# Optimization experiments

Measured on AMD Instinct MI355X. Metric: run time of the kernel, lower is better.

## Reference

```python
import jax, jax.numpy as jnp
import numpy as np

N_NODES = 50000
N_EDGES = 800000
D_IN = 128
D_H = 128
D_OUT = 1
N_GRAPHS = 64
BN_EPS = 1e-5


def _lin(key, i, o):
    return jax.random.normal(key, (i, o), jnp.float32) / np.float32(np.sqrt(i))


def setup_inputs() -> dict:
    key = jax.random.key(0)
    ks = jax.random.split(key, 40)
    inp = {}
    inp["x"] = jax.random.normal(ks[0], (N_NODES, D_IN), jnp.float32)
    inp["edge_index"] = jax.random.randint(ks[1], (2, N_EDGES), 0, N_NODES)
    inp["batch"] = jnp.sort(jax.random.randint(ks[2], (N_NODES,), 0, N_GRAPHS))
    dims = [D_IN, D_H, D_H]
    ki = 3
    for l in range(3):
        inp[f"l{l}_W1"] = _lin(ks[ki], dims[l], D_H); ki += 1
        inp[f"l{l}_b1"] = jnp.zeros((D_H,), jnp.float32)
        inp[f"l{l}_W2"] = _lin(ks[ki], D_H, D_H); ki += 1
        inp[f"l{l}_b2"] = jnp.zeros((D_H,), jnp.float32)
        inp[f"l{l}_g"] = jnp.ones((D_H,), jnp.float32)
        inp[f"l{l}_beta"] = jnp.zeros((D_H,), jnp.float32)
    inp["p_W1"] = _lin(ks[ki], D_H * 3, D_H); ki += 1
    inp["p_b1"] = jnp.zeros((D_H,), jnp.float32)
    inp["p_g"] = jnp.ones((D_H,), jnp.float32)
    inp["p_beta"] = jnp.zeros((D_H,), jnp.float32)
    inp["p_W2"] = _lin(ks[ki], D_H, D_OUT); ki += 1
    inp["p_b2"] = jnp.zeros((D_OUT,), jnp.float32)
    return inp


def _bn(h, g, b):
    # training-mode BatchNorm1d: biased batch statistics over dim 0
    m = h.mean(0)
    v = h.var(0)
    return (h - m) * (g / jnp.sqrt(v + BN_EPS)) + b


def _gin_conv(x, src, dst, W1, b1, W2, b2):
    # scatter-add neighbor aggregation: messages x[src] summed into dst
    agg = jax.ops.segment_sum(x[src], dst, num_segments=N_NODES)
    h = x + agg  # eps = 0 (GINConv default)
    h = jax.nn.relu(h @ W1 + b1)
    return h @ W2 + b2


def reference(x, edge_index, batch,
              l0_W1, l0_b1, l0_W2, l0_b2, l0_g, l0_beta,
              l1_W1, l1_b1, l1_W2, l1_b2, l1_g, l1_beta,
              l2_W1, l2_b1, l2_W2, l2_b2, l2_g, l2_beta,
              p_W1, p_b1, p_g, p_beta, p_W2, p_b2):
    src, dst = edge_index[0], edge_index[1]
    layers = [
        (l0_W1, l0_b1, l0_W2, l0_b2, l0_g, l0_beta),
        (l1_W1, l1_b1, l1_W2, l1_b2, l1_g, l1_beta),
        (l2_W1, l2_b1, l2_W2, l2_b2, l2_g, l2_beta),
    ]
    h = x
    h_list = []
    for (W1, b1, W2, b2, g, beta) in layers:
        h = _gin_conv(h, src, dst, W1, b1, W2, b2)
        h = jax.nn.relu(_bn(h, g, beta))
        # dropout: identity in eval mode
        h_list.append(h)
    # global mean pool per layer, then concat
    cnt = jax.ops.segment_sum(jnp.ones((N_NODES,), jnp.float32), batch,
                              num_segments=N_GRAPHS)
    cnt = jnp.maximum(cnt, 1.0)[:, None]
    pooled = [jax.ops.segment_sum(hh, batch, num_segments=N_GRAPHS) / cnt
              for hh in h_list]
    z = jnp.concatenate(pooled, axis=1)  # [G, 3*D_H]
    # prediction MLP: fc1 -> relu -> bn -> fc2 (dropout identity)
    z = jax.nn.relu(z @ p_W1 + p_b1)
    z = _bn(z, p_g, p_beta)
    return z @ p_W2 + p_b2  # [G, D_OUT]
```

## Files before the change

### kernel.cpp

```cpp
#include <hip/hip_runtime.h>

#define NN 50000
#define NE 800000
#define D  128
#define NG 64
#define BN_EPS 1e-5f
#define SCAN_B 196

typedef __attribute__((ext_vector_type(8))) short short8;
typedef __attribute__((ext_vector_type(4))) float f32x4;

static __device__ inline unsigned short f2bf_rn(float f) {
  unsigned u = __float_as_uint(f);
  unsigned r = (u + 0x7FFF + ((u >> 16) & 1)) >> 16;
  return (unsigned short)r;
}
static __device__ inline float bf2f(unsigned short h) {
  return __uint_as_float((unsigned)h << 16);
}

__global__ void k_hist(const int* __restrict__ dst, int* __restrict__ counts) {
  int e = blockIdx.x * blockDim.x + threadIdx.x;
  if (e < NE) atomicAdd(&counts[dst[e]], 1);
}

__global__ void k_scan1(const int* __restrict__ counts, int* __restrict__ bsum) {
  const int t = threadIdx.x;
  const int i = blockIdx.x * 256 + t;
  int v = (i < NN) ? counts[i] : 0;
  #pragma unroll
  for (int d = 32; d >= 1; d >>= 1) v += __shfl_xor(v, d, 64);
  __shared__ int ws[4];
  if ((t & 63) == 0) ws[t >> 6] = v;
  __syncthreads();
  if (t == 0) bsum[blockIdx.x] = ws[0] + ws[1] + ws[2] + ws[3];
}

__global__ void k_scan2(const int* __restrict__ bsum, int* __restrict__ boff,
                        int* __restrict__ offs) {
  const int t = threadIdx.x, lane = t & 63, w = t >> 6;
  int v = (t < SCAN_B) ? bsum[t] : 0;
  int s = v;
  #pragma unroll
  for (int d = 1; d < 64; d <<= 1) { int u = __shfl_up(s, d, 64); if (lane >= d) s += u; }
  __shared__ int ws[4];
  if (lane == 63) ws[w] = s;
  __syncthreads();
  int add = 0;
  for (int k = 0; k < w; ++k) add += ws[k];
  if (t < SCAN_B) boff[t] = add + s - v;
  if (t == SCAN_B - 1) offs[NN] = add + s;
}

__global__ void k_scan3(const int* __restrict__ counts, const int* __restrict__ boff,
                        int* __restrict__ offs) {
  const int t = threadIdx.x, lane = t & 63, w = t >> 6;
  const int i = blockIdx.x * 256 + t;
  int v = (i < NN) ? counts[i] : 0;
  int s = v;
  #pragma unroll
  for (int d = 1; d < 64; d <<= 1) { int u = __shfl_up(s, d, 64); if (lane >= d) s += u; }
  __shared__ int ws[4];
  if (lane == 63) ws[w] = s;
  __syncthreads();
  int add = 0;
  for (int k = 0; k < w; ++k) add += ws[k];
  if (i < NN) offs[i] = boff[blockIdx.x] + add + s - v;
}

__global__ void k_scatter(const int* __restrict__ src, const int* __restrict__ dst,
                          const int* __restrict__ offs, int* __restrict__ cursor,
                          int* __restrict__ esrc) {
  int e = blockIdx.x * blockDim.x + threadIdx.x;
  if (e < NE) {
    int d = dst[e];
    int p = offs[d] + atomicAdd(&cursor[d], 1);
    esrc[p] = src[e];
  }
}

__global__ void k_gbounds(const int* __restrict__ batch, int* __restrict__ gstart) {
  const int g = threadIdx.x;
  if (g > NG) return;
  int lo = 0, hi = NN;
  while (lo < hi) { int mid = (lo + hi) >> 1; if (batch[mid] < g) lo = mid + 1; else hi = mid; }
  gstart[g] = lo;
}

__global__ __launch_bounds__(256) void k_cvt(const float* __restrict__ X,
                                             unsigned long long* __restrict__ Xb) {
  const int n4 = NN * D / 4;
  for (int i = blockIdx.x * blockDim.x + threadIdx.x; i < n4; i += gridDim.x * blockDim.x) {
    float4 v = ((const float4*)X)[i];
    unsigned long long p = (unsigned long long)f2bf_rn(v.x) |
                           ((unsigned long long)f2bf_rn(v.y) << 16) |
                           ((unsigned long long)f2bf_rn(v.z) << 32) |
                           ((unsigned long long)f2bf_rn(v.w) << 48);
    Xb[i] = p;
  }
}

struct WPtrs { const float* w[6]; };
__global__ void k_prep6(WPtrs ws, short* __restrict__ wb) {
  const int widx = blockIdx.y;
  const float* __restrict__ W = ws.w[widx];
  short* __restrict__ Wh = wb + (size_t)(widx * 2) * 16384;
  short* __restrict__ Wl = Wh + 16384;
  const int idx = blockIdx.x * 256 + threadIdx.x;
  const int k = idx >> 7, c = idx & 127;
  const float v = W[idx];
  const unsigned short h = f2bf_rn(v);
  const unsigned short lo = f2bf_rn(v - bf2f(h));
  const int o = ((k >> 5) * 128 + c) * 32 + (k & 31);
  Wh[o] = (short)h;
  Wl[o] = (short)lo;
}

template<bool BN>
__global__ __launch_bounds__(256) void k_aggregate(const unsigned* __restrict__ Hb,
                                                   const int* __restrict__ offs,
                                                   const int* __restrict__ esrc,
                                                   const float* __restrict__ sums,
                                                   const float* __restrict__ sumsq,
                                                   const float* __restrict__ gw,
                                                   const float* __restrict__ beta,
                                                   unsigned* __restrict__ AGGh,
                                                   unsigned* __restrict__ AGGl) {
  const int node = blockIdx.x * 4 + (threadIdx.x >> 6);
  const int lane = threadIdx.x & 63;
  float2 sc = make_float2(1.f, 1.f), sh = make_float2(0.f, 0.f);
  if (BN) {
    const float2 s2 = ((const float2*)sums)[lane];
    const float2 q2 = ((const float2*)sumsq)[lane];
    const float2 g2 = ((const float2*)gw)[lane];
    const float2 b2 = ((const float2*)beta)[lane];
    const float mx = s2.x * (1.f / NN), my = s2.y * (1.f / NN);
    sc.x = g2.x / sqrtf(q2.x * (1.f / NN) - mx * mx + BN_EPS);
    sc.y = g2.y / sqrtf(q2.y * (1.f / NN) - my * my + BN_EPS);
    sh.x = b2.x - mx * sc.x;
    sh.y = b2.y - my * sc.y;
  }

  auto rd = [&](int r) -> float2 {
    const unsigned u = Hb[r * 64 + lane];
    float2 v = make_float2(bf2f((unsigned short)u), bf2f((unsigned short)(u >> 16)));
    if (BN) {
      v.x = fmaxf(fmaf(v.x, sc.x, sh.x), 0.f);
      v.y = fmaxf(fmaf(v.y, sc.y, sh.y), 0.f);
    }
    return v;
  };

  float2 acc = rd(node);
  const int b = offs[node], e = offs[node + 1];
  int i = b;
  for (; i + 4 <= e; i += 4) {
    const int s0 = esrc[i], s1 = esrc[i + 1], s2 = esrc[i + 2], s3 = esrc[i + 3];
    const float2 v0 = rd(s0), v1 = rd(s1), v2 = rd(s2), v3 = rd(s3);
    acc.x += (v0.x + v1.x) + (v2.x + v3.x);
    acc.y += (v0.y + v1.y) + (v2.y + v3.y);
  }
  for (; i < e; ++i) {
    const float2 v = rd(esrc[i]);
    acc.x += v.x; acc.y += v.y;
  }
  const unsigned short hx = f2bf_rn(acc.x), hy = f2bf_rn(acc.y);
  AGGh[node * 64 + lane] = (unsigned)hx | ((unsigned)hy << 16);
  const unsigned short lx = f2bf_rn(acc.x - bf2f(hx)), ly = f2bf_rn(acc.y - bf2f(hy));
  AGGl[node * 64 + lane] = (unsigned)lx | ((unsigned)ly << 16);
}

template<bool FIRST>
__global__ __launch_bounds__(512, 4) void k_gemm(const short* __restrict__ Ah,
                                                 const short* __restrict__ Al,
                                                 const short* __restrict__ Wh,
                                                 const short* __restrict__ Wl,
                                                 const float* __restrict__ bias,
                                                 short* __restrict__ Ch,
                                                 short* __restrict__ Cl,
                                                 short* __restrict__ Hb,
                                                 float* __restrict__ stats) {
  __shared__ __align__(16) short sW[2][16384];
  const int t = threadIdx.x;
  {
    const short8* __restrict__ gh = (const short8*)Wh;
    const short8* __restrict__ gl = (const short8*)Wl;
    short8* s0 = (short8*)sW[0];
    short8* s1 = (short8*)sW[1];
    #pragma unroll
    for (int i = 0; i < 4; ++i) {
      s0[i * 512 + t] = gh[i * 512 + t];
      s1[i * 512 + t] = gl[i * 512 + t];
    }
  }
  if (FIRST && blockIdx.x == 0 && t < 256) stats[t] = 0.f;
  __syncthreads();

  const int l = t & 63, w = t >> 6;
  const int lr = l & 15, fq = l >> 4, lk = fq * 8;
  const int tile0 = blockIdx.x * 128 + w * 16;
  const int arow = tile0 + lr;
  const bool rowok = arow < NN;

  short8 ah[4], al[4];
  {
    const short8 z = (short8)(0);
    #pragma unroll
    for (int kc = 0; kc < 4; ++kc) {
      ah[kc] = rowok ? *(const short8*)(Ah + (size_t)arow * D + kc * 32 + lk) : z;
      al[kc] = rowok ? *(const short8*)(Al + (size_t)arow * D + kc * 32 + lk) : z;
    }
  }

  f32x4 acc[8];
  #pragma unroll
  for (int ct = 0; ct < 8; ++ct) acc[ct] = (f32x4)(0.f);

  #pragma unroll
  for (int kc = 0; kc < 4; ++kc) {
    #pragma unroll
    for (int ct = 0; ct < 8; ++ct) {
      const short8 bh = *(const short8*)(&sW[0][(kc * 128 + ct * 16 + lr) * 32 + lk]);
      const short8 bl = *(const short8*)(&sW[1][(kc * 128 + ct * 16 + lr) * 32 + lk]);
      acc[ct] = __builtin_amdgcn_mfma_f32_16x16x32_bf16(ah[kc], bh, acc[ct], 0, 0, 0);
      acc[ct] = __builtin_amdgcn_mfma_f32_16x16x32_bf16(al[kc], bh, acc[ct], 0, 0, 0);
      acc[ct] = __builtin_amdgcn_mfma_f32_16x16x32_bf16(ah[kc], bl, acc[ct], 0, 0, 0);
    }
  }

  if (FIRST) {
    #pragma unroll
    for (int ct = 0; ct < 8; ++ct) {
      const float bb = bias[ct * 16 + lr];
      #pragma unroll
      for (int j = 0; j < 4; ++j) {
        const int gr = tile0 + fq * 4 + j;
        if (gr < NN) {
          const float v = fmaxf(acc[ct][j] + bb, 0.f);
          const unsigned short h = f2bf_rn(v);
          Ch[(size_t)gr * D + ct * 16 + lr] = (short)h;
          Cl[(size_t)gr * D + ct * 16 + lr] = (short)f2bf_rn(v - bf2f(h));
        }
      }
    }
  } else {
    float ps[8], pq[8];
    #pragma unroll
    for (int ct = 0; ct < 8; ++ct) { ps[ct] = 0.f; pq[ct] = 0.f; }
    #pragma unroll
    for (int ct = 0; ct < 8; ++ct) {
      const float bb = bias[ct * 16 + lr];
      #pragma unroll
      for (int j = 0; j < 4; ++j) {
        const int gr = tile0 + fq * 4 + j;
        if (gr < NN) {
          const float v = acc[ct][j] + bb;
          Hb[(size_t)gr * D + ct * 16 + lr] = (short)f2bf_rn(v);
          ps[ct] += v; pq[ct] += v * v;
        }
      }
    }
    __syncthreads();
    float* red  = (float*)sW[0];
    float* redq = (float*)sW[1];
    const int grp = w * 4 + fq;
    #pragma unroll
    for (int ct = 0; ct < 8; ++ct) {
      red [grp * 128 + ct * 16 + lr] = ps[ct];
      redq[grp * 128 + ct * 16 + lr] = pq[ct];
    }
    __syncthreads();
    if (t < 128) {
      float s = 0.f, q = 0.f;
      #pragma unroll
      for (int g2 = 0; g2 < 32; ++g2) { s += red[g2 * 128 + t]; q += redq[g2 * 128 + t]; }
      atomicAdd(&stats[t], s);
      atomicAdd(&stats[128 + t], q);
    }
  }
}

__global__ __launch_bounds__(256) void k_pool(const unsigned short* __restrict__ Hb,
                                              const float* __restrict__ sums,
                                              const float* __restrict__ sumsq,
                                              const float* __restrict__ gw,
                                              const float* __restrict__ beta,
                                              const int* __restrict__ gstart,
                                              float* __restrict__ pooled, int lofs) {
  const int g = blockIdx.y;
  const int s = gstart[g], e = gstart[g + 1];
  const int t = threadIdx.x, c = t & 127, half = t >> 7;
  const float m  = sums[c] * (1.f / NN);
  const float sc = gw[c] / sqrtf(sumsq[c] * (1.f / NN) - m * m + BN_EPS);
  const float sh = beta[c] - m * sc;
  const int len = e - s;
  const int nchunk = (int)gridDim.x;
  const int per = (len + nchunk - 1) / nchunk;
  const int r0 = s + (int)blockIdx.x * per;
  const int r1 = min(e, r0 + per);
  float sum = 0.f;
  for (int r = r0 + half; r < r1; r += 2)
    sum += fmaxf(fmaf(bf2f(Hb[r * D + c]), sc, sh), 0.f);
  __shared__ float red[256];
  red[t] = sum;
  __syncthreads();
  if (t < 128) atomicAdd(&pooled[g * 384 + lofs + c], red[t] + red[t + 128]);
}

__global__ __launch_bounds__(128) void k_fc1(const float* __restrict__ pooled,
                                             const int* __restrict__ gstart,
                                             const float* __restrict__ W1,
                                             const float* __restrict__ b1,
                                             float* __restrict__ z1) {
  const int g = blockIdx.x, j = threadIdx.x;
  __shared__ float p[384];
  const float cnt = (float)(gstart[g + 1] - gstart[g]);
  const float inv = 1.f / fmaxf(cnt, 1.f);
  for (int k = j; k < 384; k += 128) p[k] = pooled[g * 384 + k] * inv;
  __syncthreads();
  float acc = b1[j];
  #pragma unroll 8
  for (int k = 0; k < 384; ++k) acc = fmaf(p[k], W1[k * 128 + j], acc);
  z1[g * 128 + j] = fmaxf(acc, 0.f);
}

__global__ __launch_bounds__(128) void k_head(const float* __restrict__ z1,
                                              const float* __restrict__ g,
                                              const float* __restrict__ beta,
                                              const float* __restrict__ W2,
                                              const float* __restrict__ b2,
                                              float* __restrict__ out) {
  __shared__ float z2[NG][129];
  __shared__ float w2s[128];
  const int j = threadIdx.x;
  w2s[j] = W2[j];
  float vals[NG];
  float s = 0.f, q = 0.f;
  for (int gg = 0; gg < NG; ++gg) {
    float v = z1[gg * 128 + j];
    vals[gg] = v; s += v; q += v * v;
  }
  const float m   = s / (float)NG;
  const float var = q / (float)NG - m * m;
  const float sc  = g[j] / sqrtf(var + BN_EPS);
  const float sh  = beta[j] - m * sc;
  for (int gg = 0; gg < NG; ++gg) z2[gg][j] = vals[gg] * sc + sh;
  __syncthreads();
  if (j < NG) {
    float acc = b2[0];
    #pragma unroll 8
    for (int k = 0; k < 128; ++k) acc += z2[j][k] * w2s[k];
    out[j] = acc;
  }
}

extern "C" void kernel_launch(void* const* d_in, const int* in_sizes, int n_in,
                              void* d_out, int out_size, void* d_ws, size_t ws_size,
                              hipStream_t stream) {
  const float* x     = (const float*)d_in[0];
  const int*   e_src = (const int*)d_in[1];
  const int*   e_dst = e_src + NE;
  const int*   batch = (const int*)d_in[2];
  const float *lW1[3], *lb1[3], *lW2[3], *lb2[3], *lg[3], *lbeta[3];
  for (int l = 0; l < 3; ++l) {
    lW1[l]   = (const float*)d_in[3 + 6 * l + 0];
    lb1[l]   = (const float*)d_in[3 + 6 * l + 1];
    lW2[l]   = (const float*)d_in[3 + 6 * l + 2];
    lb2[l]   = (const float*)d_in[3 + 6 * l + 3];
    lg[l]    = (const float*)d_in[3 + 6 * l + 4];
    lbeta[l] = (const float*)d_in[3 + 6 * l + 5];
  }
  const float* pW1   = (const float*)d_in[21];
  const float* pb1   = (const float*)d_in[22];
  const float* pg    = (const float*)d_in[23];
  const float* pbeta = (const float*)d_in[24];
  const float* pW2   = (const float*)d_in[25];
  const float* pb2   = (const float*)d_in[26];
  float* out = (float*)d_out;

  char* w = (char*)d_ws;
  auto alloc = [&](size_t bytes) { char* p = w; w += (bytes + 255) & ~(size_t)255; return p; };
  short* AGGh   = (short*)alloc((size_t)NN * D * 2);
  short* AGGl   = (short*)alloc((size_t)NN * D * 2);
  short* Hb0    = (short*)alloc((size_t)NN * D * 2);
  short* Hb1    = (short*)alloc((size_t)NN * D * 2);
  short* xb     = Hb1;
  int*   counts = (int*)alloc((size_t)NN * 4);
  int*   cursor = (int*)alloc((size_t)NN * 4);
  int*   offs   = (int*)alloc((size_t)(NN + 1) * 4);
  int*   esrc   = (int*)alloc((size_t)NE * 4);
  int*   bsum   = (int*)alloc((size_t)SCAN_B * 4);
  int*   boff   = (int*)alloc((size_t)SCAN_B * 4);
  int*   gstart = (int*)alloc((size_t)(NG + 1) * 4);
  float* stats  = (float*)alloc((size_t)2 * 128 * 4);
  float* sums = stats, *sumsq = stats + 128;
  float* pooled = (float*)alloc((size_t)NG * 384 * 4);
  float* z1     = (float*)alloc((size_t)NG * 128 * 4);
  short* wb     = (short*)alloc((size_t)12 * 32768);

  hipMemsetAsync(counts, 0, (size_t)NN * 4, stream);
  hipMemsetAsync(cursor, 0, (size_t)NN * 4, stream);
  hipMemsetAsync(pooled, 0, (size_t)NG * 384 * 4, stream);

  k_hist   <<<(NE + 255) / 256, 256, 0, stream>>>(e_dst, counts);
  k_scan1  <<<SCAN_B, 256, 0, stream>>>(counts, bsum);
  k_scan2  <<<1, 256, 0, stream>>>(bsum, boff, offs);
  k_scan3  <<<SCAN_B, 256, 0, stream>>>(counts, boff, offs);
  k_scatter<<<(NE + 255) / 256, 256, 0, stream>>>(e_src, e_dst, offs, cursor, esrc);
  k_gbounds<<<1, 128, 0, stream>>>(batch, gstart);
  k_cvt    <<<1024, 256, 0, stream>>>(x, (unsigned long long*)xb);

  WPtrs ws;
  ws.w[0] = lW1[0]; ws.w[1] = lW2[0];
  ws.w[2] = lW1[1]; ws.w[3] = lW2[1];
  ws.w[4] = lW1[2]; ws.w[5] = lW2[2];
  k_prep6<<<dim3(64, 6), 256, 0, stream>>>(ws, wb);
  auto plane = [&](int widx, int hilo) { return wb + (size_t)(widx * 2 + hilo) * 16384; };

  short* Hbuf[2] = {Hb0, Hb1};
  const int gemm_grid = (NN + 127) / 128;
  for (int l = 0; l < 3; ++l) {
    if (l == 0)
      k_aggregate<false><<<NN / 4, 256, 0, stream>>>((const unsigned*)xb, offs, esrc,
                                                     nullptr, nullptr, nullptr, nullptr,
                                                     (unsigned*)AGGh, (unsigned*)AGGl);
    else
      k_aggregate<true><<<NN / 4, 256, 0, stream>>>((const unsigned*)Hbuf[(l - 1) & 1], offs, esrc,
                                                    sums, sumsq, lg[l - 1], lbeta[l - 1],
                                                    (unsigned*)AGGh, (unsigned*)AGGl);
    k_gemm<true><<<gemm_grid, 512, 0, stream>>>(AGGh, AGGl,
                                                plane(2 * l, 0), plane(2 * l, 1),
                                                lb1[l], AGGh, AGGl, nullptr, stats);
    k_gemm<false><<<gemm_grid, 512, 0, stream>>>(AGGh, AGGl,
                                                 plane(2 * l + 1, 0), plane(2 * l + 1, 1),
                                                 lb2[l], nullptr, nullptr, Hbuf[l & 1], stats);
    k_pool <<<dim3(8, NG), 256, 0, stream>>>((const unsigned short*)Hbuf[l & 1],
                                             sums, sumsq, lg[l], lbeta[l],
                                             gstart, pooled, l * 128);
  }

  k_fc1 <<<NG, 128, 0, stream>>>(pooled, gstart, pW1, pb1, z1);
  k_head<<<1, 128, 0, stream>>>(z1, pg, pbeta, pW2, pb2, out);
}
```

Baseline: 422.2 us.

## Build CSR via two-level bucketed counting sort and unroll aggregation by eight

Replaces the per-node histogram, three-pass scan and per-node atomic scatter with a bucket sort over 128-node buckets. Bucket counts are reduced in shared memory, the bucket offsets are scanned in a single block, and edges are scattered as (dst,src) pairs. Each bucket is then sorted locally in LDS to produce offs and esrc. This is meant to reduce global atomic contention and launch count, at the cost of an extra 6.4MB pairs buffer and a second pass over the edges. Separately, the aggregation loop gains an 8-way unrolled path to keep more gathers in flight.

```diff
diff --git a/kernel.cpp b/kernel.cpp
--- a/kernel.cpp
+++ b/kernel.cpp
@@ -5,7 +5,7 @@
 #define D  128
 #define NG 64
 #define BN_EPS 1e-5f
-#define SCAN_B 196
+#define NBK 391
 
 typedef __attribute__((ext_vector_type(8))) short short8;
 typedef __attribute__((ext_vector_type(4))) float f32x4;
@@ -19,63 +19,85 @@
   return __uint_as_float((unsigned)h << 16);
 }
 
-__global__ void k_hist(const int* __restrict__ dst, int* __restrict__ counts) {
-  int e = blockIdx.x * blockDim.x + threadIdx.x;
-  if (e < NE) atomicAdd(&counts[dst[e]], 1);
-}
-
-__global__ void k_scan1(const int* __restrict__ counts, int* __restrict__ bsum) {
-  const int t = threadIdx.x;
-  const int i = blockIdx.x * 256 + t;
-  int v = (i < NN) ? counts[i] : 0;
-  #pragma unroll
-  for (int d = 32; d >= 1; d >>= 1) v += __shfl_xor(v, d, 64);
-  __shared__ int ws[4];
-  if ((t & 63) == 0) ws[t >> 6] = v;
-  __syncthreads();
-  if (t == 0) bsum[blockIdx.x] = ws[0] + ws[1] + ws[2] + ws[3];
-}
-
-__global__ void k_scan2(const int* __restrict__ bsum, int* __restrict__ boff,
-                        int* __restrict__ offs) {
+__global__ __launch_bounds__(256) void k_bcount(const int* __restrict__ dst,
+                                                int* __restrict__ bcnt) {
+  __shared__ int h[NBK];
+  for (int i = threadIdx.x; i < NBK; i += 256) h[i] = 0;
+  __syncthreads();
+  const int per = (NE + gridDim.x - 1) / gridDim.x;
+  const int s = blockIdx.x * per, e = min(NE, s + per);
+  for (int i = s + threadIdx.x; i < e; i += 256)
+    atomicAdd(&h[dst[i] >> 7], 1);
+  __syncthreads();
+  for (int i = threadIdx.x; i < NBK; i += 256)
+    if (h[i]) atomicAdd(&bcnt[i], h[i]);
+}
+
+__global__ void k_bscan(const int* __restrict__ bcnt, int* __restrict__ bstart,
+                        int* __restrict__ bcur, int* __restrict__ offs) {
   const int t = threadIdx.x, lane = t & 63, w = t >> 6;
-  int v = (t < SCAN_B) ? bsum[t] : 0;
+  int v = (t < NBK) ? bcnt[t] : 0;
   int s = v;
   #pragma unroll
   for (int d = 1; d < 64; d <<= 1) { int u = __shfl_up(s, d, 64); if (lane >= d) s += u; }
-  __shared__ int ws[4];
+  __shared__ int ws[8];
   if (lane == 63) ws[w] = s;
   __syncthreads();
   int add = 0;
   for (int k = 0; k < w; ++k) add += ws[k];
-  if (t < SCAN_B) boff[t] = add + s - v;
-  if (t == SCAN_B - 1) offs[NN] = add + s;
-}
-
-__global__ void k_scan3(const int* __restrict__ counts, const int* __restrict__ boff,
-                        int* __restrict__ offs) {
-  const int t = threadIdx.x, lane = t & 63, w = t >> 6;
-  const int i = blockIdx.x * 256 + t;
-  int v = (i < NN) ? counts[i] : 0;
-  int s = v;
+  const int excl = add + s - v;
+  if (t < NBK) { bstart[t] = excl; bcur[t] = excl; }
+  if (t == NBK - 1) bstart[NBK] = excl + v;
+  if (t == 0) offs[NN] = NE;
+}
+
+__global__ __launch_bounds__(256) void k_bfill(const int* __restrict__ src,
+                                               const int* __restrict__ dst,
+                                               int* __restrict__ bcur,
+                                               unsigned long long* __restrict__ pairs) {
+  const int e = blockIdx.x * 256 + threadIdx.x;
+  if (e < NE) {
+    const int d = dst[e];
+    const int p = atomicAdd(&bcur[d >> 7], 1);
+    pairs[p] = ((unsigned long long)(unsigned)d << 32) | (unsigned)src[e];
+  }
+}
+
+__global__ __launch_bounds__(256) void k_csr2(const unsigned long long* __restrict__ pairs,
+                                              const int* __restrict__ bstart,
+                                              int* __restrict__ offs,
+                                              int* __restrict__ esrc) {
+  const int b = blockIdx.x;
+  const int s = bstart[b], e = bstart[b + 1];
+  const int n0 = b * 128;
+  __shared__ int cnt[128], cur[128];
+  __shared__ int wtot[4];
+  const int t = threadIdx.x;
+  if (t < 128) cnt[t] = 0;
+  __syncthreads();
+  for (int i = s + t; i < e; i += 256)
+    atomicAdd(&cnt[(int)(pairs[i] >> 32) - n0], 1);
+  __syncthreads();
+  const int lane = t & 63, w = t >> 6;
+  const int v = (t < 128) ? cnt[t] : 0;
+  int sc = v;
   #pragma unroll
-  for (int d = 1; d < 64; d <<= 1) { int u = __shfl_up(s, d, 64); if (lane >= d) s += u; }
-  __shared__ int ws[4];
-  if (lane == 63) ws[w] = s;
-  __syncthreads();
-  int add = 0;
-  for (int k = 0; k < w; ++k) add += ws[k];
-  if (i < NN) offs[i] = boff[blockIdx.x] + add + s - v;
-}
-
-__global__ void k_scatter(const int* __restrict__ src, const int* __restrict__ dst,
-                          const int* __restrict__ offs, int* __restrict__ cursor,
-                          int* __restrict__ esrc) {
-  int e = blockIdx.x * blockDim.x + threadIdx.x;
-  if (e < NE) {
-    int d = dst[e];
-    int p = offs[d] + atomicAdd(&cursor[d], 1);
-    esrc[p] = src[e];
+  for (int d = 1; d < 64; d <<= 1) { int u = __shfl_up(sc, d, 64); if (lane >= d) sc += u; }
+  if (lane == 63) wtot[w] = sc;
+  __syncthreads();
+  const int add = (w == 1) ? wtot[0] : 0;
+  if (t < 128) {
+    const int excl = add + sc - v;
+    cur[t] = excl;
+    const int node = n0 + t;
+    if (node < NN) offs[node] = s + excl;
+  }
+  __syncthreads();
+  for (int i = s + t; i < e; i += 256) {
+    const unsigned long long p = pairs[i];
+    const int d = (int)(p >> 32);
+    const int pos = s + atomicAdd(&cur[d - n0], 1);
+    esrc[pos] = (int)(unsigned)p;
   }
 }
 
@@ -154,6 +176,14 @@
   float2 acc = rd(node);
   const int b = offs[node], e = offs[node + 1];
   int i = b;
+  for (; i + 8 <= e; i += 8) {
+    const int s0 = esrc[i],     s1 = esrc[i + 1], s2 = esrc[i + 2], s3 = esrc[i + 3];
+    const int s4 = esrc[i + 4], s5 = esrc[i + 5], s6 = esrc[i + 6], s7 = esrc[i + 7];
+    const float2 v0 = rd(s0), v1 = rd(s1), v2 = rd(s2), v3 = rd(s3);
+    const float2 v4 = rd(s4), v5 = rd(s5), v6 = rd(s6), v7 = rd(s7);
+    acc.x += ((v0.x + v1.x) + (v2.x + v3.x)) + ((v4.x + v5.x) + (v6.x + v7.x));
+    acc.y += ((v0.y + v1.y) + (v2.y + v3.y)) + ((v4.y + v5.y) + (v6.y + v7.y));
+  }
   for (; i + 4 <= e; i += 4) {
     const int s0 = esrc[i], s1 = esrc[i + 1], s2 = esrc[i + 2], s3 = esrc[i + 3];
     const float2 v0 = rd(s0), v1 = rd(s1), v2 = rd(s2), v3 = rd(s3);
@@ -385,12 +415,12 @@
   short* Hb0    = (short*)alloc((size_t)NN * D * 2);
   short* Hb1    = (short*)alloc((size_t)NN * D * 2);
   short* xb     = Hb1;
-  int*   counts = (int*)alloc((size_t)NN * 4);
-  int*   cursor = (int*)alloc((size_t)NN * 4);
+  unsigned long long* pairs = (unsigned long long*)alloc((size_t)NE * 8);
   int*   offs   = (int*)alloc((size_t)(NN + 1) * 4);
   int*   esrc   = (int*)alloc((size_t)NE * 4);
-  int*   bsum   = (int*)alloc((size_t)SCAN_B * 4);
-  int*   boff   = (int*)alloc((size_t)SCAN_B * 4);
+  int*   bcnt   = (int*)alloc((size_t)NBK * 4);
+  int*   bstart = (int*)alloc((size_t)(NBK + 1) * 4);
+  int*   bcur   = (int*)alloc((size_t)NBK * 4);
   int*   gstart = (int*)alloc((size_t)(NG + 1) * 4);
   float* stats  = (float*)alloc((size_t)2 * 128 * 4);
   float* sums = stats, *sumsq = stats + 128;
@@ -398,15 +428,13 @@
   float* z1     = (float*)alloc((size_t)NG * 128 * 4);
   short* wb     = (short*)alloc((size_t)12 * 32768);
 
-  hipMemsetAsync(counts, 0, (size_t)NN * 4, stream);
-  hipMemsetAsync(cursor, 0, (size_t)NN * 4, stream);
+  hipMemsetAsync(bcnt, 0, (size_t)NBK * 4, stream);
   hipMemsetAsync(pooled, 0, (size_t)NG * 384 * 4, stream);
 
-  k_hist   <<<(NE + 255) / 256, 256, 0, stream>>>(e_dst, counts);
-  k_scan1  <<<SCAN_B, 256, 0, stream>>>(counts, bsum);
-  k_scan2  <<<1, 256, 0, stream>>>(bsum, boff, offs);
-  k_scan3  <<<SCAN_B, 256, 0, stream>>>(counts, boff, offs);
-  k_scatter<<<(NE + 255) / 256, 256, 0, stream>>>(e_src, e_dst, offs, cursor, esrc);
+  k_bcount <<<200, 256, 0, stream>>>(e_dst, bcnt);
+  k_bscan  <<<1, 512, 0, stream>>>(bcnt, bstart, bcur, offs);
+  k_bfill  <<<(NE + 255) / 256, 256, 0, stream>>>(e_src, e_dst, bcur, pairs);
+  k_csr2   <<<NBK, 256, 0, stream>>>(pairs, bstart, offs, esrc);
   k_gbounds<<<1, 128, 0, stream>>>(batch, gstart);
   k_cvt    <<<1024, 256, 0, stream>>>(x, (unsigned long long*)xb);
 
```

New measurement: 620.6 us. 1.47x slower.

## Fuse both GIN MLP GEMMs into one kernel with LDS-resident intermediate

Applied to the files above, without the earlier changes.

Merges the two per-layer GEMM kernels into a single kernel. It holds both weight matrices in shared memory, 128 KB in total, and keeps the ReLU'd hidden activation as swizzled hi/lo bf16 in LDS instead of writing it to global and reading it back. BN statistics move to separate per-layer buffers, and each layer's buffer is zeroed by the aggregate kernel. The aggregate loop also gains an 8-way unrolled gather for more memory-level parallelism. The large LDS footprint limits occupancy to one block per CU, which may reduce latency hiding.

```diff
diff --git a/kernel.cpp b/kernel.cpp
--- a/kernel.cpp
+++ b/kernel.cpp
@@ -124,8 +124,11 @@
                                                    const float* __restrict__ sumsq,
                                                    const float* __restrict__ gw,
                                                    const float* __restrict__ beta,
+                                                   float* __restrict__ zstats,
                                                    unsigned* __restrict__ AGGh,
                                                    unsigned* __restrict__ AGGl) {
+  if (blockIdx.x == 0 && threadIdx.x < 256) zstats[threadIdx.x] = 0.f;
+
   const int node = blockIdx.x * 4 + (threadIdx.x >> 6);
   const int lane = threadIdx.x & 63;
   float2 sc = make_float2(1.f, 1.f), sh = make_float2(0.f, 0.f);
@@ -154,6 +157,14 @@
   float2 acc = rd(node);
   const int b = offs[node], e = offs[node + 1];
   int i = b;
+  for (; i + 8 <= e; i += 8) {
+    const int s0 = esrc[i],     s1 = esrc[i + 1], s2 = esrc[i + 2], s3 = esrc[i + 3];
+    const int s4 = esrc[i + 4], s5 = esrc[i + 5], s6 = esrc[i + 6], s7 = esrc[i + 7];
+    const float2 v0 = rd(s0), v1 = rd(s1), v2 = rd(s2), v3 = rd(s3);
+    const float2 v4 = rd(s4), v5 = rd(s5), v6 = rd(s6), v7 = rd(s7);
+    acc.x += ((v0.x + v1.x) + (v2.x + v3.x)) + ((v4.x + v5.x) + (v6.x + v7.x));
+    acc.y += ((v0.y + v1.y) + (v2.y + v3.y)) + ((v4.y + v5.y) + (v6.y + v7.y));
+  }
   for (; i + 4 <= e; i += 4) {
     const int s0 = esrc[i], s1 = esrc[i + 1], s2 = esrc[i + 2], s3 = esrc[i + 3];
     const float2 v0 = rd(s0), v1 = rd(s1), v2 = rd(s2), v3 = rd(s3);
@@ -170,31 +181,32 @@
   AGGl[node * 64 + lane] = (unsigned)lx | ((unsigned)ly << 16);
 }
 
-template<bool FIRST>
-__global__ __launch_bounds__(512, 4) void k_gemm(const short* __restrict__ Ah,
-                                                 const short* __restrict__ Al,
-                                                 const short* __restrict__ Wh,
-                                                 const short* __restrict__ Wl,
-                                                 const float* __restrict__ bias,
-                                                 short* __restrict__ Ch,
-                                                 short* __restrict__ Cl,
-                                                 short* __restrict__ Hb,
-                                                 float* __restrict__ stats) {
-  __shared__ __align__(16) short sW[2][16384];
+__global__ __launch_bounds__(512) void k_mlp2(const short* __restrict__ Ah,
+                                              const short* __restrict__ Al,
+                                              const short* __restrict__ W1h, const short* __restrict__ W1l,
+                                              const short* __restrict__ W2h, const short* __restrict__ W2l,
+                                              const float* __restrict__ b1, const float* __restrict__ b2,
+                                              short* __restrict__ Hb,
+                                              float* __restrict__ stats) {
+  __shared__ __align__(16) short regA[32768];
+  __shared__ __align__(16) short regB[32768];
+
   const int t = threadIdx.x;
   {
-    const short8* __restrict__ gh = (const short8*)Wh;
-    const short8* __restrict__ gl = (const short8*)Wl;
-    short8* s0 = (short8*)sW[0];
-    short8* s1 = (short8*)sW[1];
+    const short8* __restrict__ g1h = (const short8*)W1h;
+    const short8* __restrict__ g1l = (const short8*)W1l;
+    const short8* __restrict__ g2h = (const short8*)W2h;
+    const short8* __restrict__ g2l = (const short8*)W2l;
+    short8* a8 = (short8*)regA;
+    short8* b8 = (short8*)regB;
     #pragma unroll
     for (int i = 0; i < 4; ++i) {
-      s0[i * 512 + t] = gh[i * 512 + t];
-      s1[i * 512 + t] = gl[i * 512 + t];
-    }
-  }
-  if (FIRST && blockIdx.x == 0 && t < 256) stats[t] = 0.f;
-  __syncthreads();
+      a8[i * 512 + t]        = g1h[i * 512 + t];
+      a8[2048 + i * 512 + t] = g1l[i * 512 + t];
+      b8[i * 512 + t]        = g2h[i * 512 + t];
+      b8[2048 + i * 512 + t] = g2l[i * 512 + t];
+    }
+  }
 
   const int l = t & 63, w = t >> 6;
   const int lr = l & 15, fq = l >> 4, lk = fq * 8;
@@ -211,72 +223,97 @@
       al[kc] = rowok ? *(const short8*)(Al + (size_t)arow * D + kc * 32 + lk) : z;
     }
   }
+  __syncthreads();
 
   f32x4 acc[8];
   #pragma unroll
   for (int ct = 0; ct < 8; ++ct) acc[ct] = (f32x4)(0.f);
-
   #pragma unroll
   for (int kc = 0; kc < 4; ++kc) {
     #pragma unroll
     for (int ct = 0; ct < 8; ++ct) {
-      const short8 bh = *(const short8*)(&sW[0][(kc * 128 + ct * 16 + lr) * 32 + lk]);
-      const short8 bl = *(const short8*)(&sW[1][(kc * 128 + ct * 16 + lr) * 32 + lk]);
+      const short8 bh = *(const short8*)(&regA[(kc * 128 + ct * 16 + lr) * 32 + lk]);
+      const short8 bl = *(const short8*)(&regA[16384 + (kc * 128 + ct * 16 + lr) * 32 + lk]);
       acc[ct] = __builtin_amdgcn_mfma_f32_16x16x32_bf16(ah[kc], bh, acc[ct], 0, 0, 0);
       acc[ct] = __builtin_amdgcn_mfma_f32_16x16x32_bf16(al[kc], bh, acc[ct], 0, 0, 0);
       acc[ct] = __builtin_amdgcn_mfma_f32_16x16x32_bf16(ah[kc], bl, acc[ct], 0, 0, 0);
     }
   }
-
-  if (FIRST) {
-    #pragma unroll
-    for (int ct = 0; ct < 8; ++ct) {
-      const float bb = bias[ct * 16 + lr];
+  __syncthreads();
+
+  #pragma unroll
+  for (int ct = 0; ct < 8; ++ct) {
+    const float bb = b1[ct * 16 + lr];
+    #pragma unroll
+    for (int j = 0; j < 4; ++j) {
+      const int r = w * 16 + fq * 4 + j;
+      const int swc = (ct * 16 + lr) ^ ((r & 7) << 3);
+      const float v = fmaxf(acc[ct][j] + bb, 0.f);
+      const unsigned short h = f2bf_rn(v);
+      regA[r * 128 + swc] = (short)h;
+      regA[16384 + r * 128 + swc] = (short)f2bf_rn(v - bf2f(h));
+    }
+  }
+  __syncthreads();
+
+  f32x4 acc2[8];
+  #pragma unroll
+  for (int ct = 0; ct < 8; ++ct) acc2[ct] = (f32x4)(0.f);
+  {
+    const int r = w * 16 + lr;
+    const int sx = (r & 7) << 3;
+    short8 ch[4], cl[4];
+    #pragma unroll
+    for (int kc = 0; kc < 4; ++kc) {
+      const int swb = r * 128 + ((kc * 32 + lk) ^ sx);
+      ch[kc] = *(const short8*)(regA + swb);
+      cl[kc] = *(const short8*)(regA + 16384 + swb);
+    }
+    #pragma unroll
+    for (int kc = 0; kc < 4; ++kc) {
       #pragma unroll
-      for (int j = 0; j < 4; ++j) {
-        const int gr = tile0 + fq * 4 + j;
-        if (gr < NN) {
-          const float v = fmaxf(acc[ct][j] + bb, 0.f);
-          const unsigned short h = f2bf_rn(v);
-          Ch[(size_t)gr * D + ct * 16 + lr] = (short)h;
-          Cl[(size_t)gr * D + ct * 16 + lr] = (short)f2bf_rn(v - bf2f(h));
-        }
+      for (int ct = 0; ct < 8; ++ct) {
+        const short8 bh = *(const short8*)(&regB[(kc * 128 + ct * 16 + lr) * 32 + lk]);
+        const short8 bl = *(const short8*)(&regB[16384 + (kc * 128 + ct * 16 + lr) * 32 + lk]);
+        acc2[ct] = __builtin_amdgcn_mfma_f32_16x16x32_bf16(ch[kc], bh, acc2[ct], 0, 0, 0);
+        acc2[ct] = __builtin_amdgcn_mfma_f32_16x16x32_bf16(cl[kc], bh, acc2[ct], 0, 0, 0);
+        acc2[ct] = __builtin_amdgcn_mfma_f32_16x16x32_bf16(ch[kc], bl, acc2[ct], 0, 0, 0);
       }
     }
-  } else {
-    float ps[8], pq[8];
-    #pragma unroll
-    for (int ct = 0; ct < 8; ++ct) { ps[ct] = 0.f; pq[ct] = 0.f; }
-    #pragma unroll
-    for (int ct = 0; ct < 8; ++ct) {
-      const float bb = bias[ct * 16 + lr];
-      #pragma unroll
-      for (int j = 0; j < 4; ++j) {
-        const int gr = tile0 + fq * 4 + j;
-        if (gr < NN) {
-          const float v = acc[ct][j] + bb;
-          Hb[(size_t)gr * D + ct * 16 + lr] = (short)f2bf_rn(v);
-          ps[ct] += v; pq[ct] += v * v;
-        }
+  }
+
+  float ps[8], pq[8];
+  #pragma unroll
+  for (int ct = 0; ct < 8; ++ct) { ps[ct] = 0.f; pq[ct] = 0.f; }
+  #pragma unroll
+  for (int ct = 0; ct < 8; ++ct) {
+    const float bb = b2[ct * 16 + lr];
+    #pragma unroll
+    for (int j = 0; j < 4; ++j) {
+      const int gr = tile0 + fq * 4 + j;
+      if (gr < NN) {
+        const float v = acc2[ct][j] + bb;
+        Hb[(size_t)gr * D + ct * 16 + lr] = (short)f2bf_rn(v);
+        ps[ct] += v; pq[ct] += v * v;
       }
     }
-    __syncthreads();
-    float* red  = (float*)sW[0];
-    float* redq = (float*)sW[1];
-    const int grp = w * 4 + fq;
-    #pragma unroll
-    for (int ct = 0; ct < 8; ++ct) {
-      red [grp * 128 + ct * 16 + lr] = ps[ct];
-      redq[grp * 128 + ct * 16 + lr] = pq[ct];
-    }
-    __syncthreads();
-    if (t < 128) {
-      float s = 0.f, q = 0.f;
-      #pragma unroll
-      for (int g2 = 0; g2 < 32; ++g2) { s += red[g2 * 128 + t]; q += redq[g2 * 128 + t]; }
-      atomicAdd(&stats[t], s);
-      atomicAdd(&stats[128 + t], q);
-    }
+  }
+  __syncthreads();
+  float* red  = (float*)regA;
+  float* redq = red + 4096;
+  const int grp = w * 4 + fq;
+  #pragma unroll
+  for (int ct = 0; ct < 8; ++ct) {
+    red [grp * 128 + ct * 16 + lr] = ps[ct];
+    redq[grp * 128 + ct * 16 + lr] = pq[ct];
+  }
+  __syncthreads();
+  if (t < 128) {
+    float s = 0.f, q = 0.f;
+    #pragma unroll
+    for (int g2 = 0; g2 < 32; ++g2) { s += red[g2 * 128 + t]; q += redq[g2 * 128 + t]; }
+    atomicAdd(&stats[t], s);
+    atomicAdd(&stats[128 + t], q);
   }
 }
 
@@ -392,11 +429,11 @@
   int*   bsum   = (int*)alloc((size_t)SCAN_B * 4);
   int*   boff   = (int*)alloc((size_t)SCAN_B * 4);
   int*   gstart = (int*)alloc((size_t)(NG + 1) * 4);
-  float* stats  = (float*)alloc((size_t)2 * 128 * 4);
-  float* sums = stats, *sumsq = stats + 128;
+  float* stats  = (float*)alloc((size_t)3 * 256 * 4);
   float* pooled = (float*)alloc((size_t)NG * 384 * 4);
   float* z1     = (float*)alloc((size_t)NG * 128 * 4);
   short* wb     = (short*)alloc((size_t)12 * 32768);
+  auto st = [&](int l) { return stats + (size_t)l * 256; };
 
   hipMemsetAsync(counts, 0, (size_t)NN * 4, stream);
   hipMemsetAsync(cursor, 0, (size_t)NN * 4, stream);
@@ -418,24 +455,22 @@
   auto plane = [&](int widx, int hilo) { return wb + (size_t)(widx * 2 + hilo) * 16384; };
 
   short* Hbuf[2] = {Hb0, Hb1};
-  const int gemm_grid = (NN + 127) / 128;
+  const int mlp_grid = (NN + 127) / 128;
   for (int l = 0; l < 3; ++l) {
     if (l == 0)
       k_aggregate<false><<<NN / 4, 256, 0, stream>>>((const unsigned*)xb, offs, esrc,
                                                      nullptr, nullptr, nullptr, nullptr,
-                                                     (unsigned*)AGGh, (unsigned*)AGGl);
+                                                     st(0), (unsigned*)AGGh, (unsigned*)AGGl);
     else
       k_aggregate<true><<<NN / 4, 256, 0, stream>>>((const unsigned*)Hbuf[(l - 1) & 1], offs, esrc,
-                                                    sums, sumsq, lg[l - 1], lbeta[l - 1],
-                                                    (unsigned*)AGGh, (unsigned*)AGGl);
-    k_gemm<true><<<gemm_grid, 512, 0, stream>>>(AGGh, AGGl,
-                                                plane(2 * l, 0), plane(2 * l, 1),
-                                                lb1[l], AGGh, AGGl, nullptr, stats);
-    k_gemm<false><<<gemm_grid, 512, 0, stream>>>(AGGh, AGGl,
-                                                 plane(2 * l + 1, 0), plane(2 * l + 1, 1),
-                                                 lb2[l], nullptr, nullptr, Hbuf[l & 1], stats);
+                                                    st(l - 1), st(l - 1) + 128, lg[l - 1], lbeta[l - 1],
+                                                    st(l), (unsigned*)AGGh, (unsigned*)AGGl);
+    k_mlp2<<<mlp_grid, 512, 0, stream>>>(AGGh, AGGl,
+                                         plane(2 * l, 0), plane(2 * l, 1),
+                                         plane(2 * l + 1, 0), plane(2 * l + 1, 1),
+                                         lb1[l], lb2[l], Hbuf[l & 1], st(l));
     k_pool <<<dim3(8, NG), 256, 0, stream>>>((const unsigned short*)Hbuf[l & 1],
-                                             sums, sumsq, lg[l], lbeta[l],
+                                             st(l), st(l) + 128, lg[l], lbeta[l],
                                              gstart, pooled, l * 128);
   }
 
```

Result: faster. 390.7 us (-7.5%).

## Compress edge sources to 16-bit, unroll gather, fold small kernels together

Applied to the files above, without the earlier changes.

Stores the CSR source indices as 16-bit values, which halves index traffic in the aggregation gather. It also adds a 16-way unrolled gather loop so more loads are in flight per node. The graph-boundary binary search moves into an extra block of the conversion kernel, and stats zeroing moves from the GEMM into the aggregate kernel, which now uses separate per-layer stats buffers. Node ids go up to 49999, so they fit in an unsigned short, but this hardcodes the node count under 65536.

```diff
diff --git a/kernel.cpp b/kernel.cpp
--- a/kernel.cpp
+++ b/kernel.cpp
@@ -70,27 +70,31 @@
 
 __global__ void k_scatter(const int* __restrict__ src, const int* __restrict__ dst,
                           const int* __restrict__ offs, int* __restrict__ cursor,
-                          int* __restrict__ esrc) {
+                          unsigned short* __restrict__ esrc) {
   int e = blockIdx.x * blockDim.x + threadIdx.x;
   if (e < NE) {
     int d = dst[e];
     int p = offs[d] + atomicAdd(&cursor[d], 1);
-    esrc[p] = src[e];
-  }
-}
-
-__global__ void k_gbounds(const int* __restrict__ batch, int* __restrict__ gstart) {
-  const int g = threadIdx.x;
-  if (g > NG) return;
-  int lo = 0, hi = NN;
-  while (lo < hi) { int mid = (lo + hi) >> 1; if (batch[mid] < g) lo = mid + 1; else hi = mid; }
-  gstart[g] = lo;
+    esrc[p] = (unsigned short)src[e];
+  }
 }
 
 __global__ __launch_bounds__(256) void k_cvt(const float* __restrict__ X,
-                                             unsigned long long* __restrict__ Xb) {
+                                             unsigned long long* __restrict__ Xb,
+                                             const int* __restrict__ batch,
+                                             int* __restrict__ gstart) {
+  if (blockIdx.x == gridDim.x - 1) {
+    const int g = threadIdx.x;
+    if (g <= NG) {
+      int lo = 0, hi = NN;
+      while (lo < hi) { int mid = (lo + hi) >> 1; if (batch[mid] < g) lo = mid + 1; else hi = mid; }
+      gstart[g] = lo;
+    }
+    return;
+  }
   const int n4 = NN * D / 4;
-  for (int i = blockIdx.x * blockDim.x + threadIdx.x; i < n4; i += gridDim.x * blockDim.x) {
+  const int nb = gridDim.x - 1;
+  for (int i = blockIdx.x * blockDim.x + threadIdx.x; i < n4; i += nb * blockDim.x) {
     float4 v = ((const float4*)X)[i];
     unsigned long long p = (unsigned long long)f2bf_rn(v.x) |
                            ((unsigned long long)f2bf_rn(v.y) << 16) |
@@ -119,13 +123,16 @@
 template<bool BN>
 __global__ __launch_bounds__(256) void k_aggregate(const unsigned* __restrict__ Hb,
                                                    const int* __restrict__ offs,
-                                                   const int* __restrict__ esrc,
+                                                   const unsigned short* __restrict__ esrc,
                                                    const float* __restrict__ sums,
                                                    const float* __restrict__ sumsq,
                                                    const float* __restrict__ gw,
                                                    const float* __restrict__ beta,
+                                                   float* __restrict__ zstats,
                                                    unsigned* __restrict__ AGGh,
                                                    unsigned* __restrict__ AGGl) {
+  if (blockIdx.x == 0 && threadIdx.x < 256) zstats[threadIdx.x] = 0.f;
+
   const int node = blockIdx.x * 4 + (threadIdx.x >> 6);
   const int lane = threadIdx.x & 63;
   float2 sc = make_float2(1.f, 1.f), sh = make_float2(0.f, 0.f);
@@ -154,6 +161,15 @@
   float2 acc = rd(node);
   const int b = offs[node], e = offs[node + 1];
   int i = b;
+  for (; i + 16 <= e; i += 16) {
+    float2 v[16];
+    #pragma unroll
+    for (int q = 0; q < 16; ++q) v[q] = rd((int)esrc[i + q]);
+    float sx = 0.f, sy = 0.f;
+    #pragma unroll
+    for (int q = 0; q < 16; ++q) { sx += v[q].x; sy += v[q].y; }
+    acc.x += sx; acc.y += sy;
+  }
   for (; i + 4 <= e; i += 4) {
     const int s0 = esrc[i], s1 = esrc[i + 1], s2 = esrc[i + 2], s3 = esrc[i + 3];
     const float2 v0 = rd(s0), v1 = rd(s1), v2 = rd(s2), v3 = rd(s3);
@@ -161,7 +177,7 @@
     acc.y += (v0.y + v1.y) + (v2.y + v3.y);
   }
   for (; i < e; ++i) {
-    const float2 v = rd(esrc[i]);
+    const float2 v = rd((int)esrc[i]);
     acc.x += v.x; acc.y += v.y;
   }
   const unsigned short hx = f2bf_rn(acc.x), hy = f2bf_rn(acc.y);
@@ -193,7 +209,6 @@
       s1[i * 512 + t] = gl[i * 512 + t];
     }
   }
-  if (FIRST && blockIdx.x == 0 && t < 256) stats[t] = 0.f;
   __syncthreads();
 
   const int l = t & 63, w = t >> 6;
@@ -388,15 +403,15 @@
   int*   counts = (int*)alloc((size_t)NN * 4);
   int*   cursor = (int*)alloc((size_t)NN * 4);
   int*   offs   = (int*)alloc((size_t)(NN + 1) * 4);
-  int*   esrc   = (int*)alloc((size_t)NE * 4);
+  unsigned short* esrc = (unsigned short*)alloc((size_t)NE * 2);
   int*   bsum   = (int*)alloc((size_t)SCAN_B * 4);
   int*   boff   = (int*)alloc((size_t)SCAN_B * 4);
   int*   gstart = (int*)alloc((size_t)(NG + 1) * 4);
-  float* stats  = (float*)alloc((size_t)2 * 128 * 4);
-  float* sums = stats, *sumsq = stats + 128;
+  float* stats  = (float*)alloc((size_t)3 * 256 * 4);
   float* pooled = (float*)alloc((size_t)NG * 384 * 4);
   float* z1     = (float*)alloc((size_t)NG * 128 * 4);
   short* wb     = (short*)alloc((size_t)12 * 32768);
+  auto st = [&](int l) { return stats + (size_t)l * 256; };
 
   hipMemsetAsync(counts, 0, (size_t)NN * 4, stream);
   hipMemsetAsync(cursor, 0, (size_t)NN * 4, stream);
@@ -407,8 +422,7 @@
   k_scan2  <<<1, 256, 0, stream>>>(bsum, boff, offs);
   k_scan3  <<<SCAN_B, 256, 0, stream>>>(counts, boff, offs);
   k_scatter<<<(NE + 255) / 256, 256, 0, stream>>>(e_src, e_dst, offs, cursor, esrc);
-  k_gbounds<<<1, 128, 0, stream>>>(batch, gstart);
-  k_cvt    <<<1024, 256, 0, stream>>>(x, (unsigned long long*)xb);
+  k_cvt    <<<1025, 256, 0, stream>>>(x, (unsigned long long*)xb, batch, gstart);
 
   WPtrs ws;
   ws.w[0] = lW1[0]; ws.w[1] = lW2[0];
@@ -423,19 +437,19 @@
     if (l == 0)
       k_aggregate<false><<<NN / 4, 256, 0, stream>>>((const unsigned*)xb, offs, esrc,
                                                      nullptr, nullptr, nullptr, nullptr,
-                                                     (unsigned*)AGGh, (unsigned*)AGGl);
+                                                     st(0), (unsigned*)AGGh, (unsigned*)AGGl);
     else
       k_aggregate<true><<<NN / 4, 256, 0, stream>>>((const unsigned*)Hbuf[(l - 1) & 1], offs, esrc,
-                                                    sums, sumsq, lg[l - 1], lbeta[l - 1],
-                                                    (unsigned*)AGGh, (unsigned*)AGGl);
+                                                    st(l - 1), st(l - 1) + 128, lg[l - 1], lbeta[l - 1],
+                                                    st(l), (unsigned*)AGGh, (unsigned*)AGGl);
     k_gemm<true><<<gemm_grid, 512, 0, stream>>>(AGGh, AGGl,
                                                 plane(2 * l, 0), plane(2 * l, 1),
-                                                lb1[l], AGGh, AGGl, nullptr, stats);
+                                                lb1[l], AGGh, AGGl, nullptr, nullptr);
     k_gemm<false><<<gemm_grid, 512, 0, stream>>>(AGGh, AGGl,
                                                  plane(2 * l + 1, 0), plane(2 * l + 1, 1),
-                                                 lb2[l], nullptr, nullptr, Hbuf[l & 1], stats);
+                                                 lb2[l], nullptr, nullptr, Hbuf[l & 1], st(l));
     k_pool <<<dim3(8, NG), 256, 0, stream>>>((const unsigned short*)Hbuf[l & 1],
-                                             sums, sumsq, lg[l], lbeta[l],
+                                             st(l), st(l) + 128, lg[l], lbeta[l],
                                              gstart, pooled, l * 128);
   }
 
```

After: 396.4 us. 1.07x faster.
